# Optimization experiments

Hardware: AMD Instinct MI355X
Metric: run time of the kernel (lower is better)

Reference implementation:

```python
import jax, jax.numpy as jnp
import numpy as np


def setup_inputs() -> dict:
    key = jax.random.key(0)
    k1, k2 = jax.random.split(key)
    N, C, D, Hg, Wg = 2, 12, 8, 16, 16
    H, W = 1024, 1024
    grid = jax.random.normal(k1, (N, C, D, Hg, Wg), dtype=jnp.float32)
    guidemap = jax.random.uniform(k2, (N, 1, H, W), dtype=jnp.float32)
    return {"grid": grid, "guidemap": guidemap}


def reference(grid, guidemap):
    # Bilateral grid slicing: 3D trilinear grid_sample, padding='border', align_corners=True.
    # grid: [N, C, D, Hg, Wg]; guidemap: [N, 1, H, W] -> out: [N, C, H, W]
    N, C, D, Hg, Wg = grid.shape
    _, _, H, W = guidemap.shape

    # Normalized sample coords in [-1, 1] (meshgrid over output pixels).
    yn = jnp.linspace(-1.0, 1.0, H)                      # [H]
    xn = jnp.linspace(-1.0, 1.0, W)                      # [W]
    zn = guidemap[:, 0] * 2.0 - 1.0                      # [N, H, W]

    # Unnormalize (align_corners=True) and clamp to border.
    iy = jnp.clip((yn + 1.0) * 0.5 * (Hg - 1), 0.0, Hg - 1.0)  # [H]
    ix = jnp.clip((xn + 1.0) * 0.5 * (Wg - 1), 0.0, Wg - 1.0)  # [W]
    iz = jnp.clip((zn + 1.0) * 0.5 * (D - 1), 0.0, D - 1.0)    # [N, H, W]

    iy0 = jnp.floor(iy).astype(jnp.int32)
    ix0 = jnp.floor(ix).astype(jnp.int32)
    iy1 = jnp.minimum(iy0 + 1, Hg - 1)
    ix1 = jnp.minimum(ix0 + 1, Wg - 1)
    wy = (iy - iy0)[:, None]                              # [H, 1]
    wx = (ix - ix0)[None, :]                              # [1, W]

    Y0, Y1 = iy0[:, None], iy1[:, None]                   # [H, 1]
    X0, X1 = ix0[None, :], ix1[None, :]                   # [1, W]

    iz0 = jnp.floor(iz).astype(jnp.int32)                 # [N, H, W]
    iz1 = jnp.minimum(iz0 + 1, D - 1)
    wz = iz - iz0                                         # [N, H, W]

    def sample_one(g, z0, z1, wzn):
        # g: [C, D, Hg, Wg]; z0, z1, wzn: [H, W]
        def gat(zz, yy, xx):
            return g[:, zz, yy, xx]                       # [C, H, W]
        # interpolate along z first, then x, then y
        c00 = gat(z0, Y0, X0) * (1.0 - wzn) + gat(z1, Y0, X0) * wzn
        c01 = gat(z0, Y0, X1) * (1.0 - wzn) + gat(z1, Y0, X1) * wzn
        c10 = gat(z0, Y1, X0) * (1.0 - wzn) + gat(z1, Y1, X0) * wzn
        c11 = gat(z0, Y1, X1) * (1.0 - wzn) + gat(z1, Y1, X1) * wzn
        c0 = c00 * (1.0 - wx) + c01 * wx
        c1 = c10 * (1.0 - wx) + c11 * wx
        return c0 * (1.0 - wy) + c1 * wy                  # [C, H, W]

    coeff = jax.vmap(sample_one)(grid, iz0, iz1, wz)      # [N, C, H, W]
    return coeff
```

## Files before the change

### kernel.cpp

```cpp
#include <hip/hip_runtime.h>

#define H 1024
#define W 1024
#define NC 12
#define ND 8
#define HG 16
#define WG 16

__global__ __launch_bounds__(256) void slice_kernel(
    const float* __restrict__ grid,
    const float* __restrict__ guide,
    float* __restrict__ out)
{
    const int y   = blockIdx.x;
    const int n   = blockIdx.y;
    const int tid = threadIdx.x;

    float yn = -1.0f + 2.0f * (float)y / (float)(H - 1);
    float iy = (yn + 1.0f) * 0.5f * (float)(HG - 1);
    iy = fminf(fmaxf(iy, 0.0f), (float)(HG - 1));
    int   iy0 = (int)floorf(iy);
    int   iy1 = min(iy0 + 1, HG - 1);
    float wy  = iy - (float)iy0;

    __shared__ __align__(16) float sg[2 * WG * ND * NC];
    const float* gbase = grid + (size_t)n * NC * ND * HG * WG;
    for (int i = tid; i < 2 * NC * ND * WG; i += 256) {
        int x  = i & (WG - 1);
        int z  = (i >> 4) & (ND - 1);
        int cy = i >> 7;
        int c  = cy % NC;
        int ys = cy / NC;
        int yy = ys ? iy1 : iy0;
        float v = gbase[((c * ND + z) * HG + yy) * WG + x];
        sg[((ys * WG + x) * ND + z) * NC + c] = v;
    }
    __syncthreads();

    const float* gd = guide + ((size_t)n * H + y) * W;
    float*       ob = out + ((size_t)n * NC * H + y) * W;

    for (int x = tid; x < W; x += 256) {
        float xn = -1.0f + 2.0f * (float)x / (float)(W - 1);
        float ix = (xn + 1.0f) * 0.5f * (float)(WG - 1);
        ix = fminf(fmaxf(ix, 0.0f), (float)(WG - 1));
        int   ix0 = (int)floorf(ix);
        int   ix1 = min(ix0 + 1, WG - 1);
        float wx  = ix - (float)ix0;

        float g  = gd[x];
        float zn = g * 2.0f - 1.0f;
        float iz = (zn + 1.0f) * 0.5f * (float)(ND - 1);
        iz = fminf(fmaxf(iz, 0.0f), (float)(ND - 1));
        int   iz0 = (int)floorf(iz);
        int   iz1 = min(iz0 + 1, ND - 1);
        float wz  = iz - (float)iz0;
        float omz = 1.0f - wz;

        int b00 = (ix0 * ND) * NC;
        int b01 = (ix1 * ND) * NC;
        int b10 = ((WG + ix0) * ND) * NC;
        int b11 = ((WG + ix1) * ND) * NC;
        int oz0 = iz0 * NC;
        int oz1 = iz1 * NC;

        float w00 = (1.0f - wy) * (1.0f - wx);
        float w01 = (1.0f - wy) * wx;
        float w10 = wy * (1.0f - wx);
        float w11 = wy * wx;

        #pragma unroll
        for (int cc = 0; cc < NC; cc += 4) {
            const float4 a00 = *(const float4*)&sg[b00 + oz0 + cc];
            const float4 b00v= *(const float4*)&sg[b00 + oz1 + cc];
            const float4 a01 = *(const float4*)&sg[b01 + oz0 + cc];
            const float4 b01v= *(const float4*)&sg[b01 + oz1 + cc];
            const float4 a10 = *(const float4*)&sg[b10 + oz0 + cc];
            const float4 b10v= *(const float4*)&sg[b10 + oz1 + cc];
            const float4 a11 = *(const float4*)&sg[b11 + oz0 + cc];
            const float4 b11v= *(const float4*)&sg[b11 + oz1 + cc];

            float r0 = (a00.x * omz + b00v.x * wz) * w00
                     + (a01.x * omz + b01v.x * wz) * w01
                     + (a10.x * omz + b10v.x * wz) * w10
                     + (a11.x * omz + b11v.x * wz) * w11;
            float r1 = (a00.y * omz + b00v.y * wz) * w00
                     + (a01.y * omz + b01v.y * wz) * w01
                     + (a10.y * omz + b10v.y * wz) * w10
                     + (a11.y * omz + b11v.y * wz) * w11;
            float r2 = (a00.z * omz + b00v.z * wz) * w00
                     + (a01.z * omz + b01v.z * wz) * w01
                     + (a10.z * omz + b10v.z * wz) * w10
                     + (a11.z * omz + b11v.z * wz) * w11;
            float r3 = (a00.w * omz + b00v.w * wz) * w00
                     + (a01.w * omz + b01v.w * wz) * w01
                     + (a10.w * omz + b10v.w * wz) * w10
                     + (a11.w * omz + b11v.w * wz) * w11;

            ob[(size_t)(cc + 0) * H * W + x] = r0;
            ob[(size_t)(cc + 1) * H * W + x] = r1;
            ob[(size_t)(cc + 2) * H * W + x] = r2;
            ob[(size_t)(cc + 3) * H * W + x] = r3;
        }
    }
}

extern "C" void kernel_launch(void* const* d_in, const int* in_sizes, int n_in,
                              void* d_out, int out_size, void* d_ws, size_t ws_size,
                              hipStream_t stream) {
    const float* grid  = (const float*)d_in[0];
    const float* guide = (const float*)d_in[1];
    float* out = (float*)d_out;

    dim3 grd(H, 2);
    dim3 blk(256);
    slice_kernel<<<grd, blk, 0, stream>>>(grid, guide, out);
}
```

Baseline: 129.3 us.

## Pre-interpolate grid along y in shared memory and vectorize per-thread pixels

```diff
diff --git a/kernel.cpp b/kernel.cpp
--- a/kernel.cpp
+++ b/kernel.cpp
@@ -23,24 +23,32 @@
     int   iy1 = min(iy0 + 1, HG - 1);
     float wy  = iy - (float)iy0;
 
-    __shared__ __align__(16) float sg[2 * WG * ND * NC];
+    __shared__ __align__(16) float sg[WG * ND * NC];
     const float* gbase = grid + (size_t)n * NC * ND * HG * WG;
-    for (int i = tid; i < 2 * NC * ND * WG; i += 256) {
+    for (int i = tid; i < WG * ND * NC; i += 256) {
         int x  = i & (WG - 1);
-        int z  = (i >> 4) & (ND - 1);
-        int cy = i >> 7;
-        int c  = cy % NC;
-        int ys = cy / NC;
-        int yy = ys ? iy1 : iy0;
-        float v = gbase[((c * ND + z) * HG + yy) * WG + x];
-        sg[((ys * WG + x) * ND + z) * NC + c] = v;
+        int zc = i >> 4;
+        int z  = zc & (ND - 1);
+        int c  = zc >> 3;
+        const float* gp = gbase + ((c * ND + z) * HG) * WG + x;
+        float r0 = gp[iy0 * WG];
+        float r1 = gp[iy1 * WG];
+        sg[(x * ND + z) * NC + c] = r0 + (r1 - r0) * wy;
     }
     __syncthreads();
 
+    const int xb = tid * 4;
     const float* gd = guide + ((size_t)n * H + y) * W;
     float*       ob = out + ((size_t)n * NC * H + y) * W;
 
-    for (int x = tid; x < W; x += 256) {
+    const float4 g4 = *(const float4*)&gd[xb];
+    const float gz[4] = {g4.x, g4.y, g4.z, g4.w};
+
+    float res[NC][4];
+
+    #pragma unroll
+    for (int p = 0; p < 4; ++p) {
+        const int x = xb + p;
         float xn = -1.0f + 2.0f * (float)x / (float)(W - 1);
         float ix = (xn + 1.0f) * 0.5f * (float)(WG - 1);
         ix = fminf(fmaxf(ix, 0.0f), (float)(WG - 1));
@@ -48,60 +56,48 @@
         int   ix1 = min(ix0 + 1, WG - 1);
         float wx  = ix - (float)ix0;
 
-        float g  = gd[x];
-        float zn = g * 2.0f - 1.0f;
+        float zn = gz[p] * 2.0f - 1.0f;
         float iz = (zn + 1.0f) * 0.5f * (float)(ND - 1);
         iz = fminf(fmaxf(iz, 0.0f), (float)(ND - 1));
         int   iz0 = (int)floorf(iz);
         int   iz1 = min(iz0 + 1, ND - 1);
         float wz  = iz - (float)iz0;
-        float omz = 1.0f - wz;
 
-        int b00 = (ix0 * ND) * NC;
-        int b01 = (ix1 * ND) * NC;
-        int b10 = ((WG + ix0) * ND) * NC;
-        int b11 = ((WG + ix1) * ND) * NC;
-        int oz0 = iz0 * NC;
-        int oz1 = iz1 * NC;
-
-        float w00 = (1.0f - wy) * (1.0f - wx);
-        float w01 = (1.0f - wy) * wx;
-        float w10 = wy * (1.0f - wx);
-        float w11 = wy * wx;
+        const int B0 = ix0 * (ND * NC);
+        const int B1 = ix1 * (ND * NC);
+        const int Z0 = iz0 * NC;
+        const int Z1 = iz1 * NC;
 
         #pragma unroll
         for (int cc = 0; cc < NC; cc += 4) {
-            const float4 a00 = *(const float4*)&sg[b00 + oz0 + cc];
-            const float4 b00v= *(const float4*)&sg[b00 + oz1 + cc];
-            const float4 a01 = *(const float4*)&sg[b01 + oz0 + cc];
-            const float4 b01v= *(const float4*)&sg[b01 + oz1 + cc];
-            const float4 a10 = *(const float4*)&sg[b10 + oz0 + cc];
-            const float4 b10v= *(const float4*)&sg[b10 + oz1 + cc];
-            const float4 a11 = *(const float4*)&sg[b11 + oz0 + cc];
-            const float4 b11v= *(const float4*)&sg[b11 + oz1 + cc];
+            const float4 a0 = *(const float4*)&sg[B0 + Z0 + cc];
+            const float4 a1 = *(const float4*)&sg[B0 + Z1 + cc];
+            const float4 b0 = *(const float4*)&sg[B1 + Z0 + cc];
+            const float4 b1 = *(const float4*)&sg[B1 + Z1 + cc];
 
-            float r0 = (a00.x * omz + b00v.x * wz) * w00
-                     + (a01.x * omz + b01v.x * wz) * w01
-                     + (a10.x * omz + b10v.x * wz) * w10
-                     + (a11.x * omz + b11v.x * wz) * w11;
-            float r1 = (a00.y * omz + b00v.y * wz) * w00
-                     + (a01.y * omz + b01v.y * wz) * w01
-                     + (a10.y * omz + b10v.y * wz) * w10
-                     + (a11.y * omz + b11v.y * wz) * w11;
-            float r2 = (a00.z * omz + b00v.z * wz) * w00
-                     + (a01.z * omz + b01v.z * wz) * w01
-                     + (a10.z * omz + b10v.z * wz) * w10
-                     + (a11.z * omz + b11v.z * wz) * w11;
-            float r3 = (a00.w * omz + b00v.w * wz) * w00
-                     + (a01.w * omz + b01v.w * wz) * w01
-                     + (a10.w * omz + b10v.w * wz) * w10
-                     + (a11.w * omz + b11v.w * wz) * w11;
+            float za, zb;
+            za = a0.x + (a1.x - a0.x) * wz;
+            zb = b0.x + (b1.x - b0.x) * wz;
+            res[cc + 0][p] = za + (zb - za) * wx;
 
-            ob[(size_t)(cc + 0) * H * W + x] = r0;
-            ob[(size_t)(cc + 1) * H * W + x] = r1;
-            ob[(size_t)(cc + 2) * H * W + x] = r2;
-            ob[(size_t)(cc + 3) * H * W + x] = r3;
+            za = a0.y + (a1.y - a0.y) * wz;
+            zb = b0.y + (b1.y - b0.y) * wz;
+            res[cc + 1][p] = za + (zb - za) * wx;
+
+            za = a0.z + (a1.z - a0.z) * wz;
+            zb = b0.z + (b1.z - b0.z) * wz;
+            res[cc + 2][p] = za + (zb - za) * wx;
+
+            za = a0.w + (a1.w - a0.w) * wz;
+            zb = b0.w + (b1.w - b0.w) * wz;
+            res[cc + 3][p] = za + (zb - za) * wx;
         }
+    }
+
+    #pragma unroll
+    for (int c = 0; c < NC; ++c) {
+        float4 v = make_float4(res[c][0], res[c][1], res[c][2], res[c][3]);
+        *(float4*)&ob[(size_t)c * H * W + xb] = v;
     }
 }
 
```

Result: faster. 122.0 us (-5.6%).
